# Kernel optimization log

Hardware: AMD Instinct MI355X
Metric: run time of the kernel (lower is better)

## Reference

```python
import jax, jax.numpy as jnp
import numpy as np

NX, NY, NM, NDT, NU, ND = 128, 64, 32, 32, 32, 32
N_STEPS, B, TP = 1024, 128, 64


def _spectral_weight(U, sig, V, smin, smax):
    # W = U @ diag(sigma_clamped) @ V with sigma in [smin, smax];
    # spectral (orthogonality) error penalizes non-orthogonal U, V.
    s = smin + (smax - smin) * jax.nn.sigmoid(sig)
    nin, nout = U.shape[0], V.shape[0]
    k = s.shape[0]
    Sigma = jnp.zeros((nin, nout), U.dtype).at[jnp.arange(k), jnp.arange(k)].set(s)
    W = U @ Sigma @ V
    err = jnp.mean((U @ U.T - jnp.eye(nin, dtype=U.dtype)) ** 2) \
        + jnp.mean((V @ V.T - jnp.eye(nout, dtype=V.dtype)) ** 2)
    return W, err


def _pf_weight(w, scal, smin, smax):
    # Perron-Frobenius interval weight: column-stochastic (softmax over rows)
    # scaled elementwise into [smin, smax].
    s = smax - (smax - smin) * jax.nn.sigmoid(scal)
    return s * jax.nn.softmax(w, axis=0)


def setup_inputs() -> dict:
    key = jax.random.key(0)
    ks = jax.random.split(key, 20)
    f = lambda i, sh, sc=1.0: jax.random.normal(ks[i], sh, jnp.float32) * sc
    u = lambda i, sh: jax.random.uniform(ks[i], sh, jnp.float32)
    inp = {
        # forward data args
        "Ym": f(0, (TP, B, NY)),
        "M_flow": u(1, (N_STEPS, B, NM)),
        "DT": u(2, (N_STEPS, B, NDT)),
        "D": u(3, (N_STEPS, B, ND)),
        "XMIN": jnp.zeros((N_STEPS, B, NX), jnp.float32),
        "XMAX": jnp.ones((N_STEPS, B, NX), jnp.float32),
        "UMIN": jnp.zeros((N_STEPS, B, NU), jnp.float32),
        "UMAX": jnp.ones((N_STEPS, B, NU), jnp.float32),
        # learned parameters
        "x0_correct": jnp.zeros((1, NX), jnp.float32),
        "U_A": f(4, (NX, NX), 0.1), "sig_A": u(5, (NX,)), "V_A": f(6, (NX, NX), 0.1),
        "U_C": f(7, (NX, NX), 0.1), "sig_C": u(8, (NY,)), "V_C": f(9, (NY, NY), 0.1),
        "w_E": u(10, (ND, NX)), "s_E": u(11, (ND, NX)),
        "w_B": f(12, (NU, NX), 0.1),
        "W_hf": f(13, (NU, NM, NDT), 0.1),
        "W_ih": f(14, (NY, NX), 0.1), "W_hh": f(15, (NX, NX), 0.1),
        # non-trainable buffers
        "dxmin": -0.5 * jnp.ones((1, NX), jnp.float32),
        "dxmax": 0.5 * jnp.ones((1, NX), jnp.float32),
    }
    return inp


def _forward(Ym, M_flow, DT, D, XMIN, XMAX, UMIN, UMAX, x0_correct,
             U_A, sig_A, V_A, U_C, sig_C, V_C, w_E, s_E, w_B, W_hf,
             W_ih, W_hh, dxmin, dxmax):
    W_A, errA = _spectral_weight(U_A, sig_A, V_A, 0.1, 0.9)   # state transition, sigma in [0.1,0.9]
    W_C, errC = _spectral_weight(U_C, sig_C, V_C, 0.9, 1.0)   # output map, sigma in [0.9,1]
    W_E = _pf_weight(w_E, s_E, 0.05, 1.0)                      # disturbance map
    W_Bpos = jax.nn.relu(w_B)                                  # non-negative input map
    spect_err = errA + errC

    # RNN state estimator over past observations; x0 = last hidden output
    def rnn_step(h, y_t):
        h = jax.nn.gelu(y_t @ W_ih + h @ W_hh)
        return h, None
    h0 = jnp.zeros((Ym.shape[1], W_ih.shape[1]), Ym.dtype)
    x0, _ = jax.lax.scan(rnn_step, h0, Ym)

    def step(x, ins):
        m, dT, d, xmin, xmax, umin, umax = ins
        x_prev = x
        xc = x + x0_correct
        u = jnp.einsum('bi,oij,bj->bo', m, W_hf, dT)   # bilinear heat flow
        Bu = u @ W_Bpos
        Ed = d @ W_E
        x_new = xc @ W_A + Bu + Ed
        y = x_new @ W_C
        sxmin = jax.nn.relu(xmin - x_new)
        sxmax = jax.nn.relu(x_new - xmax)
        sumin = jax.nn.relu(umin - u)
        sumax = jax.nn.relu(u - umax)
        dx_x = x_new - x_prev
        dx_u = jax.nn.relu(dxmin - Bu) + jax.nn.relu(Bu - dxmax)
        dx_d = jax.nn.relu(dxmin - Ed) + jax.nn.relu(Ed - dxmax)
        return x_new, (x_new, y, u, sxmin, sxmax, sumin, sumax, dx_x, dx_u, dx_d)

    _, outs = jax.lax.scan(step, x0, (M_flow, DT, D, XMIN, XMAX, UMIN, UMAX))
    X, Y, U, Sxmin, Sxmax, Sumin, Sumax, Sdx_x, Sdx_u, Sdx_d = outs
    SpectErr = jnp.full((M_flow.shape[0],), spect_err)
    return (X, Y, U, Sxmin, Sxmax, Sumin, Sumax, Sdx_x, Sdx_u, Sdx_d, SpectErr)


def reference(Ym, M_flow, DT, D, XMIN, XMAX, UMIN, UMAX, x0_correct,
              U_A, sig_A, V_A, U_C, sig_C, V_C, w_E, s_E, w_B, W_hf,
              W_ih, W_hh, dxmin, dxmax):
    return _forward(Ym, M_flow, DT, D, XMIN, XMAX, UMIN, UMAX, x0_correct,
                    U_A, sig_A, V_A, U_C, sig_C, V_C, w_E, s_E, w_B, W_hf,
                    W_ih, W_hh, dxmin, dxmax)
```

## Files before the change

### kernel.cpp

```cpp
#include <hip/hip_runtime.h>
#include <math.h>


#define OUT_X      0
#define OUT_Y      16777216
#define OUT_U      25165824
#define OUT_SXMIN  29360128
#define OUT_SXMAX  46137344
#define OUT_SUMIN  62914560
#define OUT_SUMAX  67108864
#define OUT_SDXX   71303168
#define OUT_SDXU   88080384
#define OUT_SDXD   104857600
#define OUT_SPECT  121634816

#define WS_WA     0
#define WS_APOW   65536
#define WS_WC     589824
#define WS_WB     606208
#define WS_WE     614400
#define WS_WHF    622592
#define WS_R      688128
#define WS_ERRP   688640
#define WS_Z      1048576
#define WS_C      5242880
#define WS_XLOC   38797312

#define XSTR 136

typedef _Float16 half8  __attribute__((ext_vector_type(8)));
typedef _Float16 half4v __attribute__((ext_vector_type(4)));
typedef float    floatx4 __attribute__((ext_vector_type(4)));

#define MFMA16(a,b,c) __builtin_amdgcn_mfma_f32_16x16x32_f16((a),(b),(c),0,0,0)

__device__ __forceinline__ float sigm(float x){ return 1.0f/(1.0f+expf(-x)); }
__device__ __forceinline__ float gelu_t(float x){
  float u = 0.7978845608028654f*(x + 0.044715f*x*x*x);
  return 0.5f*x*(1.0f+tanhf(u));
}
__device__ __forceinline__ half8 ldg8h(const float* p){
  const floatx4* p4 = (const floatx4*)p;
  floatx4 a = p4[0], b = p4[1];
  half8 r;
  r[0]=(_Float16)a[0]; r[1]=(_Float16)a[1]; r[2]=(_Float16)a[2]; r[3]=(_Float16)a[3];
  r[4]=(_Float16)b[0]; r[5]=(_Float16)b[1]; r[6]=(_Float16)b[2]; r[7]=(_Float16)b[3];
  return r;
}
__device__ __forceinline__ half8 lds8h(const float* p){
  half8 r;
  #pragma unroll
  for (int e=0;e<8;e++) r[e] = (_Float16)p[e];
  return r;
}
__device__ __forceinline__ floatx4 h4f4(half4v h){
  floatx4 f; f[0]=(float)h[0]; f[1]=(float)h[1]; f[2]=(float)h[2]; f[3]=(float)h[3]; return f;
}
__device__ __forceinline__ half4v f4h4(floatx4 f){
  half4v h; h[0]=(_Float16)f[0]; h[1]=(_Float16)f[1]; h[2]=(_Float16)f[2]; h[3]=(_Float16)f[3]; return h;
}

__global__ __launch_bounds__(256,1) void k1_weights(
    const float* __restrict__ U_A, const float* __restrict__ sig_A, const float* __restrict__ V_A,
    const float* __restrict__ U_C, const float* __restrict__ sig_C, const float* __restrict__ V_C,
    const float* __restrict__ w_E, const float* __restrict__ s_E,  const float* __restrict__ w_B,
    const float* __restrict__ W_hf,
    const float* __restrict__ Ym, const float* __restrict__ W_ih, const float* __restrict__ W_hh,
    char* __restrict__ ws)
{
  int tid = threadIdx.x, bid = blockIdx.x;

  if (bid >= 64){
    int b = bid - 64;
    __shared__ float ybAll[4096];
    __shared__ float hbuf[2][128];
    for (int e=tid; e<4096; e+=256)
      ybAll[e] = Ym[(e>>6)*8192 + b*64 + (e&63)];
    if (tid < 128) hbuf[0][tid] = 0.f;
    float wih[64], whh[128];
    if (tid < 128){
      #pragma unroll
      for (int k=0;k<64;k++)  wih[k] = W_ih[k*128+tid];
      #pragma unroll
      for (int k=0;k<128;k++) whh[k] = W_hh[k*128+tid];
    }
    __syncthreads();
    int cur = 0;
    for (int t=0;t<64;t++){
      if (tid < 128){
        const float* yb = &ybAll[t*64];
        const float* hb = hbuf[cur];
        float a0=0.f,a1=0.f,a2=0.f,a3=0.f;
        #pragma unroll
        for (int k=0;k<64;k+=4){
          a0 += yb[k]  *wih[k];   a1 += yb[k+1]*wih[k+1];
          a2 += yb[k+2]*wih[k+2]; a3 += yb[k+3]*wih[k+3];
        }
        #pragma unroll
        for (int k=0;k<128;k+=4){
          a0 += hb[k]  *whh[k];   a1 += hb[k+1]*whh[k+1];
          a2 += hb[k+2]*whh[k+2]; a3 += hb[k+3]*whh[k+3];
        }
        hbuf[cur^1][tid] = gelu_t((a0+a1)+(a2+a3));
      }
      __syncthreads();
      cur ^= 1;
    }
    if (tid < 128){
      float* z0 = (float*)(ws + WS_Z);
      z0[b*128 + tid] = hbuf[cur][tid];
    }
    return;
  }

  __shared__ float sA[128];
  __shared__ float sC[64];
  __shared__ float redw[4];
  if (tid < 128) sA[tid] = 0.1f + 0.8f*sigm(sig_A[tid]);
  else if (tid < 192) sC[tid-128] = 0.9f + 0.1f*sigm(sig_C[tid-128]);
  __syncthreads();

  float*     wa  = (float*)(ws + WS_WA);
  _Float16*  ap1 = (_Float16*)(ws + WS_APOW);
  _Float16*  wc  = (_Float16*)(ws + WS_WC);
  _Float16*  wb  = (_Float16*)(ws + WS_WB);
  _Float16*  we  = (_Float16*)(ws + WS_WE);
  _Float16*  whf = (_Float16*)(ws + WS_WHF);
  float*     errp= (float*)(ws + WS_ERRP);

  {
    int e = bid*256 + tid;
    int i = e >> 7, j = e & 127;
    float acc = 0.f;
    for (int k=0;k<128;k++) acc += U_A[i*128+k]*sA[k]*V_A[k*128+j];
    wa[i*128+j] = acc;
    ap1[j*128+i] = (_Float16)acc;
  }
  if (bid < 16){
    #pragma unroll
    for (int rep=0;rep<2;rep++){
      int e = bid*512 + rep*256 + tid;
      int i = e >> 6, n = e & 63;
      float acc = 0.f;
      for (int k=0;k<64;k++) acc += U_C[i*128+k]*sC[k]*V_C[k*64+n];
      wc[n*128+i] = (_Float16)acc;
    }
  } else if (bid == 16){
    if (tid < 128){
      int j = tid;
      float mx = -1e30f;
      for (int i=0;i<32;i++) mx = fmaxf(mx, w_E[i*128+j]);
      float ex[32]; float sm = 0.f;
      for (int i=0;i<32;i++){ ex[i] = expf(w_E[i*128+j]-mx); sm += ex[i]; }
      for (int i=0;i<32;i++){
        float s = 1.0f - 0.95f*sigm(s_E[i*128+j]);
        we[j*32+i] = (_Float16)(s*ex[i]/sm);
      }
    }
  } else if (bid == 17){
    if (tid < 128){
      int n = tid;
      for (int k=0;k<32;k++) wb[n*32+k] = (_Float16)fmaxf(w_B[k*128+n], 0.f);
    }
  } else if (bid == 18){
    for (int rep=0;rep<128;rep++){
      int e = rep*256 + tid;
      int o = e >> 10, i = (e>>5)&31, j = e & 31;
      whf[i*1024 + o*32 + j] = (_Float16)W_hf[e];
    }
  }

  {
    int wv = tid>>6, lane = tid&63;
    float part = 0.f;
    int dbase = (bid*4 + wv)*208;
    for (int l=0;l<208;l++){
      int d = dbase + l;
      const float* Mp; int i, j, K; float inv;
      if (d < 16384){ Mp=U_A; i=d>>7; j=d&127; K=128; inv=1.f/16384.f; }
      else if (d < 32768){ Mp=V_A; int dd=d-16384; i=dd>>7; j=dd&127; K=128; inv=1.f/16384.f; }
      else if (d < 49152){ Mp=U_C; int dd=d-32768; i=dd>>7; j=dd&127; K=128; inv=1.f/16384.f; }
      else { Mp=V_C; int dd=d-49152; i=dd>>6; j=dd&63; K=64; inv=1.f/4096.f; }
      float p;
      if (K == 128){
        float2 a = ((const float2*)(Mp + i*128))[lane];
        float2 b = ((const float2*)(Mp + j*128))[lane];
        p = a.x*b.x + a.y*b.y;
      } else {
        p = Mp[i*64+lane]*Mp[j*64+lane];
      }
      #pragma unroll
      for (int m=1;m<64;m<<=1) p += __shfl_xor(p, m, 64);
      float cdf = p - (i==j ? 1.f : 0.f);
      part += cdf*cdf*inv;
    }
    if (lane == 0) redw[wv] = part;
  }
  __syncthreads();
  if (tid == 0) errp[bid] = redw[0]+redw[1]+redw[2]+redw[3];
}

__global__ __launch_bounds__(256) void k1b_finalize(
    const float* __restrict__ x0c, char* __restrict__ ws, float* __restrict__ out)
{
  int tid = threadIdx.x;
  const float* errp = (const float*)(ws + WS_ERRP);
  const float* wa   = (const float*)(ws + WS_WA);
  float*       rws  = (float*)(ws + WS_R);
  __shared__ float red[64];
  if (tid < 64) red[tid] = errp[tid];
  __syncthreads();
  if (tid == 0){
    float s = 0.f;
    for (int i=0;i<64;i++) s += red[i];
    red[0] = s;
  }
  __syncthreads();
  float spect = red[0];
  for (int r = tid; r < 1024; r += 256) out[OUT_SPECT + r] = spect;
  if (tid < 128){
    float a = 0.f;
    for (int k=0;k<128;k++) a += x0c[k]*wa[k*128+tid];
    rws[tid] = a;
  }
}

__global__ __launch_bounds__(256,2) void k3_forcing(
    const float* __restrict__ Mf, const float* __restrict__ pDT, const float* __restrict__ pD,
    const float* __restrict__ pUMIN, const float* __restrict__ pUMAX,
    const float* __restrict__ pdxmin, const float* __restrict__ pdxmax,
    char* __restrict__ ws, float* __restrict__ out)
{
  int tid = threadIdx.x;
  int wave = tid>>6, lane = tid&63, l15 = lane&15, q = lane>>4;
  __shared__ __align__(16) float smemf[8960];

  if (blockIdx.x == 1024){
    if (tid >= 128) return;
    _Float16* xl2 = (_Float16*)smemf;
    const float*    wa = (const float*)(ws + WS_WA);
    const _Float16* a1 = (const _Float16*)(ws + WS_APOW);
    half8 af[4][4];
    #pragma unroll
    for (int mt=0;mt<4;mt++)
      #pragma unroll
      for (int kt=0;kt<4;kt++)
        af[mt][kt] = ldg8h(wa + (wave*64+mt*16+l15)*128 + kt*32 + q*8);
    for (int p=2;p<=16;p++){
      _Float16* dst = (_Float16*)(ws + WS_APOW + (p-1)*32768);
      for (int nt=0;nt<8;nt++){
        floatx4 acc[4];
        #pragma unroll
        for (int mt=0;mt<4;mt++){ acc[mt][0]=0.f; acc[mt][1]=0.f; acc[mt][2]=0.f; acc[mt][3]=0.f; }
        #pragma unroll
        for (int kt=0;kt<4;kt++){
          half8 bfv = *(const half8*)(a1 + (nt*16+l15)*128 + kt*32 + q*8);
          #pragma unroll
          for (int mt=0;mt<4;mt++) acc[mt] = MFMA16(af[mt][kt], bfv, acc[mt]);
        }
        #pragma unroll
        for (int mt=0;mt<4;mt++){
          half4v hv = f4h4(acc[mt]);
          int mg = wave*64 + mt*16;
          *(half4v*)(dst + (nt*16+l15)*128 + mg + q*4) = hv;
          #pragma unroll
          for (int r=0;r<4;r++) xl2[wave*(64*XSTR) + (mt*16+q*4+r)*XSTR + nt*16+l15] = hv[r];
        }
      }
      #pragma unroll
      for (int mt=0;mt<4;mt++)
        #pragma unroll
        for (int kt=0;kt<4;kt++)
          af[mt][kt] = *(const half8*)(&xl2[wave*(64*XSTR) + (mt*16+l15)*XSTR + kt*32 + q*8]);
    }
    return;
  }

  int t = blockIdx.x;
  float* mls = smemf;
  float* uls = smemf + 4224;
  float* rls = smemf + 8576;
  float* dmn = smemf + 8704;
  float* dmx = smemf + 8832;

  const float* rws = (const float*)(ws + WS_R);
  for (int e=tid; e<4096; e+=256){
    float v = Mf[t*4096 + e];
    mls[(e>>5)*33 + (e&31)] = v;
  }
  if (tid < 128){ rls[tid]=rws[tid]; dmn[tid]=pdxmin[tid]; dmx[tid]=pdxmax[tid]; }
  __syncthreads();

  int b0 = wave*32 + l15;
  int b1 = wave*32 + 16 + l15;
  half8 dtf0 = ldg8h(pDT + t*4096 + b0*32 + q*8);
  half8 dtf1 = ldg8h(pDT + t*4096 + b1*32 + q*8);
  half8 ddf0 = ldg8h(pD  + t*4096 + b0*32 + q*8);
  half8 ddf1 = ldg8h(pD  + t*4096 + b1*32 + q*8);

  const _Float16* whf = (const _Float16*)(ws + WS_WHF);
  floatx4 u00,u01,u10,u11;
  u00[0]=u00[1]=u00[2]=u00[3]=0.f; u01=u00; u10=u00; u11=u00;
  for (int i=0;i<32;i++){
    _Float16 m0 = (_Float16)mls[b0*33 + i];
    _Float16 m1 = (_Float16)mls[b1*33 + i];
    half8 a0, a1;
    #pragma unroll
    for (int e=0;e<8;e++){ a0[e] = dtf0[e]*m0; a1[e] = dtf1[e]*m1; }
    half8 bo0 = *(const half8*)(whf + i*1024 + l15*32      + q*8);
    half8 bo1 = *(const half8*)(whf + i*1024 + (16+l15)*32 + q*8);
    u00 = MFMA16(a0, bo0, u00); u01 = MFMA16(a0, bo1, u01);
    u10 = MFMA16(a1, bo0, u10); u11 = MFMA16(a1, bo1, u11);
  }
  #pragma unroll
  for (int mt=0;mt<2;mt++){
    #pragma unroll
    for (int nto=0;nto<2;nto++){
      floatx4 uacc = mt ? (nto?u11:u10) : (nto?u01:u00);
      #pragma unroll
      for (int r=0;r<4;r++){
        int b = wave*32 + mt*16 + q*4 + r;
        int o = nto*16 + l15;
        int ub = t*4096 + b*32 + o;
        float uv = uacc[r];
        __builtin_nontemporal_store(uv, &out[OUT_U + ub]);
        __builtin_nontemporal_store(fmaxf(__builtin_nontemporal_load(&pUMIN[ub])-uv, 0.f), &out[OUT_SUMIN + ub]);
        __builtin_nontemporal_store(fmaxf(uv-__builtin_nontemporal_load(&pUMAX[ub]), 0.f), &out[OUT_SUMAX + ub]);
        uls[wave*1088 + (mt*16+q*4+r)*34 + o] = uv;
      }
    }
  }
  half8 uf0 = lds8h(&uls[wave*1088 + (l15)*34 + q*8]);
  half8 uf1 = lds8h(&uls[wave*1088 + (16+l15)*34 + q*8]);

  const _Float16* wb = (const _Float16*)(ws + WS_WB);
  const _Float16* we = (const _Float16*)(ws + WS_WE);
  _Float16* cws = (_Float16*)(ws + WS_C);
  for (int nt=0; nt<8; nt++){
    half8 wbf = *(const half8*)(wb + (nt*16+l15)*32 + q*8);
    half8 wef = *(const half8*)(we + (nt*16+l15)*32 + q*8);
    floatx4 zz; zz[0]=zz[1]=zz[2]=zz[3]=0.f;
    floatx4 bu0=MFMA16(uf0, wbf, zz), bu1=MFMA16(uf1, wbf, zz);
    floatx4 ed0=MFMA16(ddf0, wef, zz), ed1=MFMA16(ddf1, wef, zz);
    int col = nt*16 + l15;
    float dn = dmn[col], dxv = dmx[col], rv = rls[col];
    #pragma unroll
    for (int mt=0;mt<2;mt++){
      floatx4 bu = mt?bu1:bu0, ed = mt?ed1:ed0;
      half4v cp;
      #pragma unroll
      for (int r=0;r<4;r++){
        int b = wave*32 + mt*16 + q*4 + r;
        int base = t*16384 + b*128 + col;
        float buv = bu[r], edv = ed[r];
        __builtin_nontemporal_store(fmaxf(dn-buv,0.f) + fmaxf(buv-dxv,0.f), &out[OUT_SDXU + base]);
        __builtin_nontemporal_store(fmaxf(dn-edv,0.f) + fmaxf(edv-dxv,0.f), &out[OUT_SDXD + base]);
        cp[r] = (_Float16)(rv + buv + edv);
      }
      *(half4v*)(cws + (((t*8 + (wave*2+mt))*8 + nt)<<8) + lane*4) = cp;
    }
  }
}

__global__ __launch_bounds__(64,1) void k5a_pass1(char* __restrict__ ws)
{
  int lane = threadIdx.x, l15 = lane&15, q = lane>>4;
  int chunk = blockIdx.x >> 3, mt_g = blockIdx.x & 7;
  const _Float16* a1   = (const _Float16*)(ws + WS_APOW);
  const _Float16* cws  = (const _Float16*)(ws + WS_C);
  _Float16*       xloc = (_Float16*)(ws + WS_XLOC);
  __shared__ _Float16 xl[16*XSTR];

  half8 bf[8][4];
  #pragma unroll
  for (int nt=0;nt<8;nt++)
    #pragma unroll
    for (int kt=0;kt<4;kt++)
      bf[nt][kt] = *(const half8*)(a1 + (nt*16+l15)*128 + kt*32 + q*8);
  half8 af[4] = {};

  int t0 = chunk*16;
  half4v cv[8];
  #pragma unroll
  for (int nt=0;nt<8;nt++)
    cv[nt] = *(const half4v*)(cws + (((t0*8+mt_g)*8+nt)<<8) + lane*4);

  for (int s=0;s<16;s++){
    int t = t0 + s;
    floatx4 acc[8];
    #pragma unroll
    for (int nt=0;nt<8;nt++) acc[nt] = h4f4(cv[nt]);
    if (s < 15){
      #pragma unroll
      for (int nt=0;nt<8;nt++)
        cv[nt] = *(const half4v*)(cws + ((((t+1)*8+mt_g)*8+nt)<<8) + lane*4);
    }
    #pragma unroll
    for (int kt=0;kt<4;kt++)
      #pragma unroll
      for (int nt=0;nt<8;nt++)
        acc[nt] = MFMA16(af[kt], bf[nt][kt], acc[nt]);
    #pragma unroll
    for (int nt=0;nt<8;nt++){
      half4v hv = f4h4(acc[nt]);
      *(half4v*)(xloc + (((t*8+mt_g)*8+nt)<<8) + lane*4) = hv;
      #pragma unroll
      for (int r=0;r<4;r++) xl[(q*4+r)*XSTR + nt*16+l15] = hv[r];
    }
    #pragma unroll
    for (int kt=0;kt<4;kt++)
      af[kt] = *(const half8*)(&xl[l15*XSTR + kt*32 + q*8]);
  }
}

__global__ __launch_bounds__(64,1) void k5b_boundary(char* __restrict__ ws)
{
  int lane = threadIdx.x, l15 = lane&15, q = lane>>4;
  int mt_g = blockIdx.x;
  const _Float16* a16  = (const _Float16*)(ws + WS_APOW + 15*32768);
  const _Float16* xloc = (const _Float16*)(ws + WS_XLOC);
  float*          z    = (float*)(ws + WS_Z);
  __shared__ _Float16 xl[16*XSTR];

  half8 bf[8][4];
  #pragma unroll
  for (int nt=0;nt<8;nt++)
    #pragma unroll
    for (int kt=0;kt<4;kt++)
      bf[nt][kt] = *(const half8*)(a16 + (nt*16+l15)*128 + kt*32 + q*8);
  half8 af[4];
  #pragma unroll
  for (int kt=0;kt<4;kt++)
    af[kt] = ldg8h(z + (mt_g*16+l15)*128 + kt*32 + q*8);

  half4v pf[8];
  #pragma unroll
  for (int nt=0;nt<8;nt++)
    pf[nt] = *(const half4v*)(xloc + (((15*8+mt_g)*8+nt)<<8) + lane*4);

  for (int c=0;c<63;c++){
    floatx4 acc[8];
    #pragma unroll
    for (int nt=0;nt<8;nt++) acc[nt] = h4f4(pf[nt]);
    if (c < 62){
      int tn = (c+1)*16 + 15;
      #pragma unroll
      for (int nt=0;nt<8;nt++)
        pf[nt] = *(const half4v*)(xloc + (((tn*8+mt_g)*8+nt)<<8) + lane*4);
    }
    #pragma unroll
    for (int kt=0;kt<4;kt++)
      #pragma unroll
      for (int nt=0;nt<8;nt++)
        acc[nt] = MFMA16(af[kt], bf[nt][kt], acc[nt]);
    #pragma unroll
    for (int nt=0;nt<8;nt++){
      #pragma unroll
      for (int r=0;r<4;r++){
        int b = mt_g*16 + q*4 + r;
        z[(c+1)*16384 + b*128 + nt*16+l15] = acc[nt][r];
        xl[(q*4+r)*XSTR + nt*16+l15] = (_Float16)acc[nt][r];
      }
    }
    #pragma unroll
    for (int kt=0;kt<4;kt++)
      af[kt] = *(const half8*)(&xl[l15*XSTR + kt*32 + q*8]);
  }
}

__global__ __launch_bounds__(256,2) void k6_epilogue(
    const float* __restrict__ pXMIN, const float* __restrict__ pXMAX,
    char* __restrict__ ws, float* __restrict__ out)
{
  int t = blockIdx.x, tid = threadIdx.x;
  int wave = tid>>6, lane = tid&63, l15 = lane&15, q = lane>>4;
  int c = t>>4, k = t&15;
  __shared__ _Float16 xl[4][32*XSTR];

  const float*    zp   = (const float*)(ws + WS_Z) + c*16384;
  const _Float16* xloc = (const _Float16*)(ws + WS_XLOC);
  const _Float16* ap1  = (const _Float16*)(ws + WS_APOW + k*32768);
  const _Float16* ap0  = (const _Float16*)(ws + WS_APOW + (k-1)*32768);

  half8 zf[2][4];
  #pragma unroll
  for (int mt=0;mt<2;mt++)
    #pragma unroll
    for (int kt=0;kt<4;kt++)
      zf[mt][kt] = ldg8h(zp + (wave*32+mt*16+l15)*128 + kt*32 + q*8);

  for (int nt=0;nt<8;nt++){
    int col = nt*16 + l15;
    floatx4 xt[2], xm[2];
    #pragma unroll
    for (int mt=0;mt<2;mt++)
      xt[mt] = h4f4(*(const half4v*)(xloc + (((t*8 + wave*2+mt)*8 + nt)<<8) + lane*4));
    #pragma unroll
    for (int kt=0;kt<4;kt++){
      half8 b1 = *(const half8*)(ap1 + (nt*16+l15)*128 + kt*32 + q*8);
      #pragma unroll
      for (int mt=0;mt<2;mt++) xt[mt] = MFMA16(zf[mt][kt], b1, xt[mt]);
    }
    if (k > 0){
      #pragma unroll
      for (int mt=0;mt<2;mt++)
        xm[mt] = h4f4(*(const half4v*)(xloc + ((((t-1)*8 + wave*2+mt)*8 + nt)<<8) + lane*4));
      #pragma unroll
      for (int kt=0;kt<4;kt++){
        half8 b0 = *(const half8*)(ap0 + (nt*16+l15)*128 + kt*32 + q*8);
        #pragma unroll
        for (int mt=0;mt<2;mt++) xm[mt] = MFMA16(zf[mt][kt], b0, xm[mt]);
      }
    } else {
      #pragma unroll
      for (int mt=0;mt<2;mt++)
        #pragma unroll
        for (int r=0;r<4;r++)
          xm[mt][r] = zp[(wave*32+mt*16+q*4+r)*128 + col];
    }
    #pragma unroll
    for (int mt=0;mt<2;mt++){
      #pragma unroll
      for (int r=0;r<4;r++){
        int b = wave*32 + mt*16 + q*4 + r;
        int base = t*16384 + b*128 + col;
        float xv = xt[mt][r];
        __builtin_nontemporal_store(xv, &out[OUT_X + base]);
        __builtin_nontemporal_store(fmaxf(__builtin_nontemporal_load(&pXMIN[base])-xv, 0.f), &out[OUT_SXMIN + base]);
        __builtin_nontemporal_store(fmaxf(xv-__builtin_nontemporal_load(&pXMAX[base]), 0.f), &out[OUT_SXMAX + base]);
        __builtin_nontemporal_store(xv - xm[mt][r], &out[OUT_SDXX + base]);
        xl[wave][(mt*16+q*4+r)*XSTR + col] = (_Float16)xv;
      }
    }
  }
  half8 xf[2][4];
  #pragma unroll
  for (int mt=0;mt<2;mt++)
    #pragma unroll
    for (int kt=0;kt<4;kt++)
      xf[mt][kt] = *(const half8*)(&xl[wave][(mt*16+l15)*XSTR + kt*32 + q*8]);
  const _Float16* wc = (const _Float16*)(ws + WS_WC);
  #pragma unroll
  for (int ny=0;ny<4;ny++){
    floatx4 ya[2];
    ya[0][0]=ya[0][1]=ya[0][2]=ya[0][3]=0.f; ya[1]=ya[0];
    #pragma unroll
    for (int kt=0;kt<4;kt++){
      half8 wcf = *(const half8*)(wc + (ny*16+l15)*128 + kt*32 + q*8);
      #pragma unroll
      for (int mt=0;mt<2;mt++) ya[mt] = MFMA16(xf[mt][kt], wcf, ya[mt]);
    }
    #pragma unroll
    for (int mt=0;mt<2;mt++)
      #pragma unroll
      for (int r=0;r<4;r++){
        int b = wave*32 + mt*16 + q*4 + r;
        __builtin_nontemporal_store(ya[mt][r], &out[OUT_Y + t*8192 + b*64 + ny*16+l15]);
      }
  }
}

extern "C" void kernel_launch(void* const* d_in, const int* in_sizes, int n_in,
                              void* d_out, int out_size, void* d_ws, size_t ws_size,
                              hipStream_t stream) {
  (void)in_sizes; (void)n_in; (void)out_size; (void)ws_size;
  const float* Ym     = (const float*)d_in[0];
  const float* M_flow = (const float*)d_in[1];
  const float* DT     = (const float*)d_in[2];
  const float* D      = (const float*)d_in[3];
  const float* XMIN   = (const float*)d_in[4];
  const float* XMAX   = (const float*)d_in[5];
  const float* UMIN   = (const float*)d_in[6];
  const float* UMAX   = (const float*)d_in[7];
  const float* x0c    = (const float*)d_in[8];
  const float* U_A    = (const float*)d_in[9];
  const float* sig_A  = (const float*)d_in[10];
  const float* V_A    = (const float*)d_in[11];
  const float* U_C    = (const float*)d_in[12];
  const float* sig_C  = (const float*)d_in[13];
  const float* V_C    = (const float*)d_in[14];
  const float* w_E    = (const float*)d_in[15];
  const float* s_E    = (const float*)d_in[16];
  const float* w_B    = (const float*)d_in[17];
  const float* W_hf   = (const float*)d_in[18];
  const float* W_ih   = (const float*)d_in[19];
  const float* W_hh   = (const float*)d_in[20];
  const float* dxmin  = (const float*)d_in[21];
  const float* dxmax  = (const float*)d_in[22];
  char*  ws  = (char*)d_ws;
  float* out = (float*)d_out;

  hipLaunchKernelGGL(k1_weights, dim3(192), dim3(256), 0, stream,
                     U_A, sig_A, V_A, U_C, sig_C, V_C, w_E, s_E, w_B, W_hf,
                     Ym, W_ih, W_hh, ws);
  hipLaunchKernelGGL(k1b_finalize, dim3(1), dim3(256), 0, stream, x0c, ws, out);
  hipLaunchKernelGGL(k3_forcing, dim3(1025), dim3(256), 0, stream,
                     M_flow, DT, D, UMIN, UMAX, dxmin, dxmax, ws, out);
  hipLaunchKernelGGL(k5a_pass1, dim3(512), dim3(64), 0, stream, ws);
  hipLaunchKernelGGL(k5b_boundary, dim3(8), dim3(64), 0, stream, ws);
  hipLaunchKernelGGL(k6_epilogue, dim3(1024), dim3(256), 0, stream, XMIN, XMAX, ws, out);
}
```

Baseline: 1.036 ms.

## Fuse scan passes into one flag-synchronised kernel and square A powers

```diff
diff --git a/kernel.cpp b/kernel.cpp
--- a/kernel.cpp
+++ b/kernel.cpp
@@ -22,9 +22,10 @@
 #define WS_WHF    622592
 #define WS_R      688128
 #define WS_ERRP   688640
+#define WS_FLAGS  692224
 #define WS_Z      1048576
-#define WS_C      5242880
-#define WS_XLOC   38797312
+#define WS_D      5242880
+#define WS_C      8388608
 
 #define XSTR 136
 
@@ -59,6 +60,10 @@
 __device__ __forceinline__ half4v f4h4(floatx4 f){
   half4v h; h[0]=(_Float16)f[0]; h[1]=(_Float16)f[1]; h[2]=(_Float16)f[2]; h[3]=(_Float16)f[3]; return h;
 }
+__device__ __forceinline__ void waitflag(const unsigned int* p, unsigned int need){
+  while (__hip_atomic_load(p, __ATOMIC_ACQUIRE, __HIP_MEMORY_SCOPE_AGENT) < need)
+    __builtin_amdgcn_s_sleep(8);
+}
 
 __global__ __launch_bounds__(256,1) void k1_weights(
     const float* __restrict__ U_A, const float* __restrict__ sig_A, const float* __restrict__ V_A,
@@ -66,7 +71,7 @@
     const float* __restrict__ w_E, const float* __restrict__ s_E,  const float* __restrict__ w_B,
     const float* __restrict__ W_hf,
     const float* __restrict__ Ym, const float* __restrict__ W_ih, const float* __restrict__ W_hh,
-    char* __restrict__ ws)
+    const float* __restrict__ x0c, char* __restrict__ ws, float* __restrict__ out)
 {
   int tid = threadIdx.x, bid = blockIdx.x;
 
@@ -116,6 +121,8 @@
   __shared__ float sA[128];
   __shared__ float sC[64];
   __shared__ float redw[4];
+  __shared__ float rede[64];
+  __shared__ int   lastf;
   if (tid < 128) sA[tid] = 0.1f + 0.8f*sigm(sig_A[tid]);
   else if (tid < 192) sC[tid-128] = 0.9f + 0.1f*sigm(sig_C[tid-128]);
   __syncthreads();
@@ -127,6 +134,8 @@
   _Float16*  we  = (_Float16*)(ws + WS_WE);
   _Float16*  whf = (_Float16*)(ws + WS_WHF);
   float*     errp= (float*)(ws + WS_ERRP);
+  float*     rws = (float*)(ws + WS_R);
+  unsigned int* k1ctr = (unsigned int*)(ws + WS_FLAGS + 512);
 
   {
     int e = bid*256 + tid;
@@ -197,31 +206,29 @@
     if (lane == 0) redw[wv] = part;
   }
   __syncthreads();
-  if (tid == 0) errp[bid] = redw[0]+redw[1]+redw[2]+redw[3];
-}
-
-__global__ __launch_bounds__(256) void k1b_finalize(
-    const float* __restrict__ x0c, char* __restrict__ ws, float* __restrict__ out)
-{
-  int tid = threadIdx.x;
-  const float* errp = (const float*)(ws + WS_ERRP);
-  const float* wa   = (const float*)(ws + WS_WA);
-  float*       rws  = (float*)(ws + WS_R);
-  __shared__ float red[64];
-  if (tid < 64) red[tid] = errp[tid];
+  if (tid == 0){
+    errp[bid] = redw[0]+redw[1]+redw[2]+redw[3];
+    __threadfence();
+    unsigned int old = __hip_atomic_fetch_add(k1ctr, 1u, __ATOMIC_ACQ_REL, __HIP_MEMORY_SCOPE_AGENT);
+    lastf = (old == 63u) ? 1 : 0;
+  }
   __syncthreads();
-  if (tid == 0){
-    float s = 0.f;
-    for (int i=0;i<64;i++) s += red[i];
-    red[0] = s;
-  }
-  __syncthreads();
-  float spect = red[0];
-  for (int r = tid; r < 1024; r += 256) out[OUT_SPECT + r] = spect;
-  if (tid < 128){
-    float a = 0.f;
-    for (int k=0;k<128;k++) a += x0c[k]*wa[k*128+tid];
-    rws[tid] = a;
+  if (lastf){
+    if (tid < 64) rede[tid] = errp[tid];
+    __syncthreads();
+    if (tid == 0){
+      float s = 0.f;
+      for (int i=0;i<64;i++) s += rede[i];
+      rede[0] = s;
+    }
+    __syncthreads();
+    float spect = rede[0];
+    for (int r = tid; r < 1024; r += 256) out[OUT_SPECT + r] = spect;
+    if (tid < 128){
+      float a = 0.f;
+      for (int k=0;k<128;k++) a += x0c[k]*wa[k*128+tid];
+      rws[tid] = a;
+    }
   }
 }
 
@@ -236,42 +243,51 @@
   __shared__ __align__(16) float smemf[8960];
 
   if (blockIdx.x == 1024){
-    if (tid >= 128) return;
     _Float16* xl2 = (_Float16*)smemf;
-    const float*    wa = (const float*)(ws + WS_WA);
-    const _Float16* a1 = (const _Float16*)(ws + WS_APOW);
+    const float*    wa   = (const float*)(ws + WS_WA);
+    _Float16*       apow = (_Float16*)(ws + WS_APOW);
     half8 af[4][4];
-    #pragma unroll
-    for (int mt=0;mt<4;mt++)
-      #pragma unroll
-      for (int kt=0;kt<4;kt++)
-        af[mt][kt] = ldg8h(wa + (wave*64+mt*16+l15)*128 + kt*32 + q*8);
-    for (int p=2;p<=16;p++){
-      _Float16* dst = (_Float16*)(ws + WS_APOW + (p-1)*32768);
-      for (int nt=0;nt<8;nt++){
-        floatx4 acc[4];
-        #pragma unroll
-        for (int mt=0;mt<4;mt++){ acc[mt][0]=0.f; acc[mt][1]=0.f; acc[mt][2]=0.f; acc[mt][3]=0.f; }
-        #pragma unroll
-        for (int kt=0;kt<4;kt++){
-          half8 bfv = *(const half8*)(a1 + (nt*16+l15)*128 + kt*32 + q*8);
-          #pragma unroll
-          for (int mt=0;mt<4;mt++) acc[mt] = MFMA16(af[mt][kt], bfv, acc[mt]);
-        }
-        #pragma unroll
-        for (int mt=0;mt<4;mt++){
-          half4v hv = f4h4(acc[mt]);
-          int mg = wave*64 + mt*16;
-          *(half4v*)(dst + (nt*16+l15)*128 + mg + q*4) = hv;
-          #pragma unroll
-          for (int r=0;r<4;r++) xl2[wave*(64*XSTR) + (mt*16+q*4+r)*XSTR + nt*16+l15] = hv[r];
-        }
-      }
+    if (tid < 128){
       #pragma unroll
       for (int mt=0;mt<4;mt++)
         #pragma unroll
         for (int kt=0;kt<4;kt++)
-          af[mt][kt] = *(const half8*)(&xl2[wave*(64*XSTR) + (mt*16+l15)*XSTR + kt*32 + q*8]);
+          af[mt][kt] = ldg8h(wa + (wave*64+mt*16+l15)*128 + kt*32 + q*8);
+    }
+    const _Float16* srcB = apow;
+    const int slots[4] = {2,4,8,16};
+    for (int sq=0; sq<4; sq++){
+      _Float16* dst = apow + (slots[sq]-1)*16384;
+      if (tid < 128){
+        for (int nt=0;nt<8;nt++){
+          floatx4 acc[4];
+          #pragma unroll
+          for (int mt=0;mt<4;mt++){ acc[mt][0]=0.f; acc[mt][1]=0.f; acc[mt][2]=0.f; acc[mt][3]=0.f; }
+          #pragma unroll
+          for (int kt=0;kt<4;kt++){
+            half8 bfv = *(const half8*)(srcB + (nt*16+l15)*128 + kt*32 + q*8);
+            #pragma unroll
+            for (int mt=0;mt<4;mt++) acc[mt] = MFMA16(af[mt][kt], bfv, acc[mt]);
+          }
+          #pragma unroll
+          for (int mt=0;mt<4;mt++){
+            half4v hv = f4h4(acc[mt]);
+            int mg = wave*64 + mt*16;
+            *(half4v*)(dst + (nt*16+l15)*128 + mg + q*4) = hv;
+            #pragma unroll
+            for (int r=0;r<4;r++) xl2[wave*(64*XSTR) + (mt*16+q*4+r)*XSTR + nt*16+l15] = hv[r];
+          }
+        }
+      }
+      __syncthreads();
+      if (tid < 128){
+        #pragma unroll
+        for (int mt=0;mt<4;mt++)
+          #pragma unroll
+          for (int kt=0;kt<4;kt++)
+            af[mt][kt] = *(const half8*)(&xl2[wave*(64*XSTR) + (mt*16+l15)*XSTR + kt*32 + q*8]);
+      }
+      srcB = dst;
     }
     return;
   }
@@ -362,201 +378,221 @@
   }
 }
 
-__global__ __launch_bounds__(64,1) void k5a_pass1(char* __restrict__ ws)
-{
-  int lane = threadIdx.x, l15 = lane&15, q = lane>>4;
-  int chunk = blockIdx.x >> 3, mt_g = blockIdx.x & 7;
-  const _Float16* a1   = (const _Float16*)(ws + WS_APOW);
-  const _Float16* cws  = (const _Float16*)(ws + WS_C);
-  _Float16*       xloc = (_Float16*)(ws + WS_XLOC);
-  __shared__ _Float16 xl[16*XSTR];
-
-  half8 bf[8][4];
-  #pragma unroll
-  for (int nt=0;nt<8;nt++)
-    #pragma unroll
-    for (int kt=0;kt<4;kt++)
-      bf[nt][kt] = *(const half8*)(a1 + (nt*16+l15)*128 + kt*32 + q*8);
-  half8 af[4] = {};
-
-  int t0 = chunk*16;
-  half4v cv[8];
-  #pragma unroll
-  for (int nt=0;nt<8;nt++)
-    cv[nt] = *(const half4v*)(cws + (((t0*8+mt_g)*8+nt)<<8) + lane*4);
-
-  for (int s=0;s<16;s++){
-    int t = t0 + s;
-    floatx4 acc[8];
-    #pragma unroll
-    for (int nt=0;nt<8;nt++) acc[nt] = h4f4(cv[nt]);
-    if (s < 15){
-      #pragma unroll
-      for (int nt=0;nt<8;nt++)
-        cv[nt] = *(const half4v*)(cws + ((((t+1)*8+mt_g)*8+nt)<<8) + lane*4);
-    }
-    #pragma unroll
-    for (int kt=0;kt<4;kt++)
-      #pragma unroll
-      for (int nt=0;nt<8;nt++)
-        acc[nt] = MFMA16(af[kt], bf[nt][kt], acc[nt]);
-    #pragma unroll
-    for (int nt=0;nt<8;nt++){
-      half4v hv = f4h4(acc[nt]);
-      *(half4v*)(xloc + (((t*8+mt_g)*8+nt)<<8) + lane*4) = hv;
-      #pragma unroll
-      for (int r=0;r<4;r++) xl[(q*4+r)*XSTR + nt*16+l15] = hv[r];
-    }
-    #pragma unroll
-    for (int kt=0;kt<4;kt++)
-      af[kt] = *(const half8*)(&xl[l15*XSTR + kt*32 + q*8]);
-  }
-}
-
-__global__ __launch_bounds__(64,1) void k5b_boundary(char* __restrict__ ws)
-{
-  int lane = threadIdx.x, l15 = lane&15, q = lane>>4;
-  int mt_g = blockIdx.x;
-  const _Float16* a16  = (const _Float16*)(ws + WS_APOW + 15*32768);
-  const _Float16* xloc = (const _Float16*)(ws + WS_XLOC);
-  float*          z    = (float*)(ws + WS_Z);
-  __shared__ _Float16 xl[16*XSTR];
-
-  half8 bf[8][4];
-  #pragma unroll
-  for (int nt=0;nt<8;nt++)
-    #pragma unroll
-    for (int kt=0;kt<4;kt++)
-      bf[nt][kt] = *(const half8*)(a16 + (nt*16+l15)*128 + kt*32 + q*8);
-  half8 af[4];
-  #pragma unroll
-  for (int kt=0;kt<4;kt++)
-    af[kt] = ldg8h(z + (mt_g*16+l15)*128 + kt*32 + q*8);
-
-  half4v pf[8];
-  #pragma unroll
-  for (int nt=0;nt<8;nt++)
-    pf[nt] = *(const half4v*)(xloc + (((15*8+mt_g)*8+nt)<<8) + lane*4);
-
-  for (int c=0;c<63;c++){
-    floatx4 acc[8];
-    #pragma unroll
-    for (int nt=0;nt<8;nt++) acc[nt] = h4f4(pf[nt]);
-    if (c < 62){
-      int tn = (c+1)*16 + 15;
-      #pragma unroll
-      for (int nt=0;nt<8;nt++)
-        pf[nt] = *(const half4v*)(xloc + (((tn*8+mt_g)*8+nt)<<8) + lane*4);
-    }
-    #pragma unroll
-    for (int kt=0;kt<4;kt++)
-      #pragma unroll
-      for (int nt=0;nt<8;nt++)
-        acc[nt] = MFMA16(af[kt], bf[nt][kt], acc[nt]);
-    #pragma unroll
-    for (int nt=0;nt<8;nt++){
-      #pragma unroll
-      for (int r=0;r<4;r++){
-        int b = mt_g*16 + q*4 + r;
-        z[(c+1)*16384 + b*128 + nt*16+l15] = acc[nt][r];
-        xl[(q*4+r)*XSTR + nt*16+l15] = (_Float16)acc[nt][r];
-      }
-    }
-    #pragma unroll
-    for (int kt=0;kt<4;kt++)
-      af[kt] = *(const half8*)(&xl[l15*XSTR + kt*32 + q*8]);
-  }
-}
-
-__global__ __launch_bounds__(256,2) void k6_epilogue(
+__global__ __launch_bounds__(512,2) void k5_mega(
     const float* __restrict__ pXMIN, const float* __restrict__ pXMAX,
     char* __restrict__ ws, float* __restrict__ out)
 {
-  int t = blockIdx.x, tid = threadIdx.x;
+  int tid = threadIdx.x, bid = blockIdx.x;
   int wave = tid>>6, lane = tid&63, l15 = lane&15, q = lane>>4;
-  int c = t>>4, k = t&15;
-  __shared__ _Float16 xl[4][32*XSTR];
-
-  const float*    zp   = (const float*)(ws + WS_Z) + c*16384;
-  const _Float16* xloc = (const _Float16*)(ws + WS_XLOC);
-  const _Float16* ap1  = (const _Float16*)(ws + WS_APOW + k*32768);
-  const _Float16* ap0  = (const _Float16*)(ws + WS_APOW + (k-1)*32768);
-
-  half8 zf[2][4];
-  #pragma unroll
-  for (int mt=0;mt<2;mt++)
+  __shared__ _Float16 xl[8][16*XSTR];
+
+  unsigned int* ddone = (unsigned int*)(ws + WS_FLAGS);
+  unsigned int* zdone = (unsigned int*)(ws + WS_FLAGS + 256);
+  const _Float16* a1  = (const _Float16*)(ws + WS_APOW);
+  const _Float16* cws = (const _Float16*)(ws + WS_C);
+  _Float16*       dws = (_Float16*)(ws + WS_D);
+
+  if (bid < 64){
+    int chunk = bid, mt = wave;
+    half8 bf[8][4];
+    #pragma unroll
+    for (int nt=0;nt<8;nt++)
+      #pragma unroll
+      for (int kt=0;kt<4;kt++)
+        bf[nt][kt] = *(const half8*)(a1 + (nt*16+l15)*128 + kt*32 + q*8);
+    half8 af[4] = {};
+    int t0 = chunk*16;
+    half4v cv[8];
+    #pragma unroll
+    for (int nt=0;nt<8;nt++)
+      cv[nt] = *(const half4v*)(cws + (((t0*8+mt)*8+nt)<<8) + lane*4);
+
+    floatx4 acc[8];
+    for (int s=0;s<16;s++){
+      #pragma unroll
+      for (int nt=0;nt<8;nt++) acc[nt] = h4f4(cv[nt]);
+      if (s < 15){
+        #pragma unroll
+        for (int nt=0;nt<8;nt++)
+          cv[nt] = *(const half4v*)(cws + ((((t0+s+1)*8+mt)*8+nt)<<8) + lane*4);
+      }
+      #pragma unroll
+      for (int kt=0;kt<4;kt++)
+        #pragma unroll
+        for (int nt=0;nt<8;nt++)
+          acc[nt] = MFMA16(af[kt], bf[nt][kt], acc[nt]);
+      if (s < 15){
+        #pragma unroll
+        for (int nt=0;nt<8;nt++){
+          half4v hv = f4h4(acc[nt]);
+          #pragma unroll
+          for (int r=0;r<4;r++) xl[wave][(q*4+r)*XSTR + nt*16+l15] = hv[r];
+        }
+        #pragma unroll
+        for (int kt=0;kt<4;kt++)
+          af[kt] = *(const half8*)(&xl[wave][l15*XSTR + kt*32 + q*8]);
+      }
+    }
+    #pragma unroll
+    for (int nt=0;nt<8;nt++)
+      *(half4v*)(dws + (((chunk*8+mt)*8+nt)<<8) + lane*4) = f4h4(acc[nt]);
+    __threadfence();
+    if (lane == 0)
+      __hip_atomic_fetch_add(&ddone[chunk], 1u, __ATOMIC_RELEASE, __HIP_MEMORY_SCOPE_AGENT);
+    return;
+  }
+
+  if (bid == 64){
+    int mt = wave;
+    const _Float16* a16 = (const _Float16*)(ws + WS_APOW + 15*32768);
+    float* z = (float*)(ws + WS_Z);
+    half8 bf[8][4];
+    #pragma unroll
+    for (int nt=0;nt<8;nt++)
+      #pragma unroll
+      for (int kt=0;kt<4;kt++)
+        bf[nt][kt] = *(const half8*)(a16 + (nt*16+l15)*128 + kt*32 + q*8);
+    half8 af[4];
     #pragma unroll
     for (int kt=0;kt<4;kt++)
-      zf[mt][kt] = ldg8h(zp + (wave*32+mt*16+l15)*128 + kt*32 + q*8);
-
-  for (int nt=0;nt<8;nt++){
-    int col = nt*16 + l15;
-    floatx4 xt[2], xm[2];
-    #pragma unroll
-    for (int mt=0;mt<2;mt++)
-      xt[mt] = h4f4(*(const half4v*)(xloc + (((t*8 + wave*2+mt)*8 + nt)<<8) + lane*4));
-    #pragma unroll
-    for (int kt=0;kt<4;kt++){
-      half8 b1 = *(const half8*)(ap1 + (nt*16+l15)*128 + kt*32 + q*8);
-      #pragma unroll
-      for (int mt=0;mt<2;mt++) xt[mt] = MFMA16(zf[mt][kt], b1, xt[mt]);
-    }
-    if (k > 0){
-      #pragma unroll
-      for (int mt=0;mt<2;mt++)
-        xm[mt] = h4f4(*(const half4v*)(xloc + ((((t-1)*8 + wave*2+mt)*8 + nt)<<8) + lane*4));
-      #pragma unroll
-      for (int kt=0;kt<4;kt++){
-        half8 b0 = *(const half8*)(ap0 + (nt*16+l15)*128 + kt*32 + q*8);
-        #pragma unroll
-        for (int mt=0;mt<2;mt++) xm[mt] = MFMA16(zf[mt][kt], b0, xm[mt]);
-      }
-    } else {
-      #pragma unroll
-      for (int mt=0;mt<2;mt++)
-        #pragma unroll
-        for (int r=0;r<4;r++)
-          xm[mt][r] = zp[(wave*32+mt*16+q*4+r)*128 + col];
-    }
-    #pragma unroll
-    for (int mt=0;mt<2;mt++){
-      #pragma unroll
-      for (int r=0;r<4;r++){
-        int b = wave*32 + mt*16 + q*4 + r;
-        int base = t*16384 + b*128 + col;
-        float xv = xt[mt][r];
-        __builtin_nontemporal_store(xv, &out[OUT_X + base]);
-        __builtin_nontemporal_store(fmaxf(__builtin_nontemporal_load(&pXMIN[base])-xv, 0.f), &out[OUT_SXMIN + base]);
-        __builtin_nontemporal_store(fmaxf(xv-__builtin_nontemporal_load(&pXMAX[base]), 0.f), &out[OUT_SXMAX + base]);
-        __builtin_nontemporal_store(xv - xm[mt][r], &out[OUT_SDXX + base]);
-        xl[wave][(mt*16+q*4+r)*XSTR + col] = (_Float16)xv;
-      }
-    }
-  }
-  half8 xf[2][4];
-  #pragma unroll
-  for (int mt=0;mt<2;mt++)
+      af[kt] = ldg8h(z + (mt*16+l15)*128 + kt*32 + q*8);
+
+    waitflag(&ddone[0], 8u);
+    half4v pf[8];
+    #pragma unroll
+    for (int nt=0;nt<8;nt++)
+      pf[nt] = *(const half4v*)(dws + (((0*8+mt)*8+nt)<<8) + lane*4);
+
+    for (int c=0;c<63;c++){
+      floatx4 acc[8];
+      #pragma unroll
+      for (int nt=0;nt<8;nt++) acc[nt] = h4f4(pf[nt]);
+      if (c < 62){
+        waitflag(&ddone[c+1], 8u);
+        #pragma unroll
+        for (int nt=0;nt<8;nt++)
+          pf[nt] = *(const half4v*)(dws + ((((c+1)*8+mt)*8+nt)<<8) + lane*4);
+      }
+      #pragma unroll
+      for (int kt=0;kt<4;kt++)
+        #pragma unroll
+        for (int nt=0;nt<8;nt++)
+          acc[nt] = MFMA16(af[kt], bf[nt][kt], acc[nt]);
+      #pragma unroll
+      for (int nt=0;nt<8;nt++){
+        #pragma unroll
+        for (int r=0;r<4;r++){
+          int b = mt*16 + q*4 + r;
+          z[(c+1)*16384 + b*128 + nt*16+l15] = acc[nt][r];
+          xl[wave][(q*4+r)*XSTR + nt*16+l15] = (_Float16)acc[nt][r];
+        }
+      }
+      #pragma unroll
+      for (int kt=0;kt<4;kt++)
+        af[kt] = *(const half8*)(&xl[wave][l15*XSTR + kt*32 + q*8]);
+      __threadfence();
+      if (lane == 0)
+        __hip_atomic_fetch_add(&zdone[c+1], 1u, __ATOMIC_RELEASE, __HIP_MEMORY_SCOPE_AGENT);
+    }
+    return;
+  }
+
+  {
+    int kb = bid - 65;
+    int t0 = kb*8, c = t0>>4;
+    int mt = wave;
+    const float* zp = (const float*)(ws + WS_Z) + c*16384;
+    const _Float16* wc = (const _Float16*)(ws + WS_WC);
+
+    half8 bf[8][4];
+    #pragma unroll
+    for (int nt=0;nt<8;nt++)
+      #pragma unroll
+      for (int kt=0;kt<4;kt++)
+        bf[nt][kt] = *(const half8*)(a1 + (nt*16+l15)*128 + kt*32 + q*8);
+
+    int ts = c*16;
+    half4v cv[8];
+    #pragma unroll
+    for (int nt=0;nt<8;nt++)
+      cv[nt] = *(const half4v*)(cws + (((ts*8+mt)*8+nt)<<8) + lane*4);
+
+    if (c > 0) waitflag(&zdone[c], 8u);
+
+    half8 af[4];
     #pragma unroll
     for (int kt=0;kt<4;kt++)
-      xf[mt][kt] = *(const half8*)(&xl[wave][(mt*16+l15)*XSTR + kt*32 + q*8]);
-  const _Float16* wc = (const _Float16*)(ws + WS_WC);
-  #pragma unroll
-  for (int ny=0;ny<4;ny++){
-    floatx4 ya[2];
-    ya[0][0]=ya[0][1]=ya[0][2]=ya[0][3]=0.f; ya[1]=ya[0];
-    #pragma unroll
-    for (int kt=0;kt<4;kt++){
-      half8 wcf = *(const half8*)(wc + (ny*16+l15)*128 + kt*32 + q*8);
-      #pragma unroll
-      for (int mt=0;mt<2;mt++) ya[mt] = MFMA16(xf[mt][kt], wcf, ya[mt]);
-    }
-    #pragma unroll
-    for (int mt=0;mt<2;mt++)
-      #pragma unroll
-      for (int r=0;r<4;r++){
-        int b = wave*32 + mt*16 + q*4 + r;
-        __builtin_nontemporal_store(ya[mt][r], &out[OUT_Y + t*8192 + b*64 + ny*16+l15]);
-      }
+      af[kt] = ldg8h(zp + (mt*16+l15)*128 + kt*32 + q*8);
+    half4v prev[8];
+    #pragma unroll
+    for (int nt=0;nt<8;nt++){
+      #pragma unroll
+      for (int r=0;r<4;r++)
+        prev[nt][r] = (_Float16)zp[(mt*16+q*4+r)*128 + nt*16+l15];
+    }
+
+    for (int tt=ts; tt<t0+8; ++tt){
+      floatx4 acc[8];
+      #pragma unroll
+      for (int nt=0;nt<8;nt++) acc[nt] = h4f4(cv[nt]);
+      if (tt+1 < t0+8){
+        #pragma unroll
+        for (int nt=0;nt<8;nt++)
+          cv[nt] = *(const half4v*)(cws + ((((tt+1)*8+mt)*8+nt)<<8) + lane*4);
+      }
+      #pragma unroll
+      for (int kt=0;kt<4;kt++)
+        #pragma unroll
+        for (int nt=0;nt<8;nt++)
+          acc[nt] = MFMA16(af[kt], bf[nt][kt], acc[nt]);
+
+      if (tt >= t0){
+        #pragma unroll
+        for (int nt=0;nt<8;nt++){
+          int col = nt*16 + l15;
+          #pragma unroll
+          for (int r=0;r<4;r++){
+            int b = mt*16 + q*4 + r;
+            int base = tt*16384 + b*128 + col;
+            float xv = acc[nt][r];
+            __builtin_nontemporal_store(xv, &out[OUT_X + base]);
+            __builtin_nontemporal_store(fmaxf(__builtin_nontemporal_load(&pXMIN[base])-xv, 0.f), &out[OUT_SXMIN + base]);
+            __builtin_nontemporal_store(fmaxf(xv-__builtin_nontemporal_load(&pXMAX[base]), 0.f), &out[OUT_SXMAX + base]);
+            __builtin_nontemporal_store(xv - (float)prev[nt][r], &out[OUT_SDXX + base]);
+            xl[wave][(q*4+r)*XSTR + col] = (_Float16)xv;
+          }
+          prev[nt] = f4h4(acc[nt]);
+        }
+        #pragma unroll
+        for (int kt=0;kt<4;kt++)
+          af[kt] = *(const half8*)(&xl[wave][l15*XSTR + kt*32 + q*8]);
+        #pragma unroll
+        for (int ny=0;ny<4;ny++){
+          floatx4 ya; ya[0]=0.f; ya[1]=0.f; ya[2]=0.f; ya[3]=0.f;
+          #pragma unroll
+          for (int kt=0;kt<4;kt++){
+            half8 wcf = *(const half8*)(wc + (ny*16+l15)*128 + kt*32 + q*8);
+            ya = MFMA16(af[kt], wcf, ya);
+          }
+          #pragma unroll
+          for (int r=0;r<4;r++){
+            int b = mt*16 + q*4 + r;
+            __builtin_nontemporal_store(ya[r], &out[OUT_Y + tt*8192 + b*64 + ny*16+l15]);
+          }
+        }
+      } else {
+        #pragma unroll
+        for (int nt=0;nt<8;nt++){
+          half4v hv = f4h4(acc[nt]);
+          #pragma unroll
+          for (int r=0;r<4;r++) xl[wave][(q*4+r)*XSTR + nt*16+l15] = hv[r];
+          prev[nt] = hv;
+        }
+        #pragma unroll
+        for (int kt=0;kt<4;kt++)
+          af[kt] = *(const half8*)(&xl[wave][l15*XSTR + kt*32 + q*8]);
+      }
+    }
   }
 }
 
@@ -590,13 +626,12 @@
   char*  ws  = (char*)d_ws;
   float* out = (float*)d_out;
 
+  hipMemsetAsync(ws + WS_FLAGS, 0, 1024, stream);
   hipLaunchKernelGGL(k1_weights, dim3(192), dim3(256), 0, stream,
                      U_A, sig_A, V_A, U_C, sig_C, V_C, w_E, s_E, w_B, W_hf,
-                     Ym, W_ih, W_hh, ws);
-  hipLaunchKernelGGL(k1b_finalize, dim3(1), dim3(256), 0, stream, x0c, ws, out);
+                     Ym, W_ih, W_hh, x0c, ws, out);
   hipLaunchKernelGGL(k3_forcing, dim3(1025), dim3(256), 0, stream,
                      M_flow, DT, D, UMIN, UMAX, dxmin, dxmax, ws, out);
-  hipLaunchKernelGGL(k5a_pass1, dim3(512), dim3(64), 0, stream, ws);
-  hipLaunchKernelGGL(k5b_boundary, dim3(8), dim3(64), 0, stream, ws);
-  hipLaunchKernelGGL(k6_epilogue, dim3(1024), dim3(256), 0, stream, XMIN, XMAX, ws, out);
-}
+  hipLaunchKernelGGL(k5_mega, dim3(193), dim3(512), 0, stream,
+                     XMIN, XMAX, ws, out);
+}
```

Result: slower. 2.651 ms (+155.8%).
